# Performance work log

Measured on AMD Instinct MI355X. Metric: run time of the kernel, lower is better.

## Reference

```python
import jax, jax.numpy as jnp
import numpy as np

R = 32          # voxel resolution (init kwarg)
EPS = 0.0       # init kwarg eps


def _norm_coords(coords):
    # coords: [B, 3, N]
    nc = coords - coords.mean(axis=2, keepdims=True)
    # L2 norm over xyz (dim=1), max over points (dim=2)
    denom = jnp.linalg.norm(nc, axis=1, keepdims=True).max(axis=2, keepdims=True) * 2.0 + EPS
    nc = nc / denom + 0.5
    return jnp.clip(nc * R, 0.0, R - 1)  # [B, 3, N] in [0, R-1]


def setup_inputs() -> dict:
    key = jax.random.key(0)
    k1, k2 = jax.random.split(key)
    features = jax.random.normal(k1, (8, 64, 65536), dtype=jnp.float32)
    coords = jax.random.normal(k2, (8, 3, 65536), dtype=jnp.float32)
    return {"features": features, "coords": coords}


def reference(features, coords):
    # features: [B, C, N], coords: [B, 3, N]
    nc = _norm_coords(coords)
    vox = jnp.round(nc).astype(jnp.int32)                      # [B, 3, N]
    flat = (vox[:, 0] * R + vox[:, 1]) * R + vox[:, 2]         # [B, N] flat voxel ids

    def per_batch(f, idx):
        # f: [C, N], idx: [N] -> scatter-mean into R^3 voxels
        sums = jax.ops.segment_sum(f.T, idx, num_segments=R ** 3)            # [R^3, C]
        cnt = jax.ops.segment_sum(jnp.ones(idx.shape, jnp.float32), idx,
                                  num_segments=R ** 3)                        # [R^3]
        return (sums / jnp.maximum(cnt, 1.0)[:, None]).T                      # [C, R^3]

    vox_feat = jax.vmap(per_batch)(features, flat)             # [B, C, R^3]
    B, C = features.shape[0], features.shape[1]
    return vox_feat.reshape(B, C, R, R, R), nc
```

## Files before the change

kernel.cpp:

```cpp
#include <hip/hip_runtime.h>
#include <hip/hip_fp16.h>

#define RR 32
#define R3 32768
#define NPTS 65536
#define NCH 64
#define NB 8


__global__ void mean1_kernel(const float* __restrict__ coords, double* __restrict__ part) {
    __shared__ double ls[3][4];
    int b = blockIdx.y, blk = blockIdx.x;
    int t = threadIdx.x;
    const float* cb = coords + (size_t)b * 3 * NPTS;
    int base = blk * 1024 + t;
    double sx = 0.0, sy = 0.0, sz = 0.0;
#pragma unroll
    for (int k = 0; k < 4; k++) {
        int n = base + k * 256;
        sx += cb[n];
        sy += cb[NPTS + n];
        sz += cb[2 * NPTS + n];
    }
    for (int off = 32; off > 0; off >>= 1) {
        sx += __shfl_down(sx, off);
        sy += __shfl_down(sy, off);
        sz += __shfl_down(sz, off);
    }
    int wave = t >> 6;
    if ((t & 63) == 0) { ls[0][wave] = sx; ls[1][wave] = sy; ls[2][wave] = sz; }
    __syncthreads();
    if (t == 0) {
        part[((size_t)b * 64 + blk) * 3 + 0] = ls[0][0] + ls[0][1] + ls[0][2] + ls[0][3];
        part[((size_t)b * 64 + blk) * 3 + 1] = ls[1][0] + ls[1][1] + ls[1][2] + ls[1][3];
        part[((size_t)b * 64 + blk) * 3 + 2] = ls[2][0] + ls[2][1] + ls[2][2] + ls[2][3];
    }
}

__global__ void mean2_kernel(const double* __restrict__ part, float* __restrict__ meanf) {
    int b = blockIdx.x, l = threadIdx.x;
    double sx = part[((size_t)b * 64 + l) * 3 + 0];
    double sy = part[((size_t)b * 64 + l) * 3 + 1];
    double sz = part[((size_t)b * 64 + l) * 3 + 2];
    for (int off = 32; off > 0; off >>= 1) {
        sx += __shfl_down(sx, off);
        sy += __shfl_down(sy, off);
        sz += __shfl_down(sz, off);
    }
    if (l == 0) {
        meanf[b * 4 + 0] = (float)(sx * (1.0 / NPTS));
        meanf[b * 4 + 1] = (float)(sy * (1.0 / NPTS));
        meanf[b * 4 + 2] = (float)(sz * (1.0 / NPTS));
    }
}

__global__ void max1_kernel(const float* __restrict__ coords,
                            const float* __restrict__ meanf,
                            float* __restrict__ partmax) {
    __shared__ float ls[4];
    int b = blockIdx.y, blk = blockIdx.x;
    int t = threadIdx.x;
    float mx = meanf[b * 4 + 0], my = meanf[b * 4 + 1], mz = meanf[b * 4 + 2];
    const float* cb = coords + (size_t)b * 3 * NPTS;
    int base = blk * 1024 + t;
    float m = 0.0f;
#pragma unroll
    for (int k = 0; k < 4; k++) {
        int n = base + k * 256;
        float dx = cb[n] - mx;
        float dy = cb[NPTS + n] - my;
        float dz = cb[2 * NPTS + n] - mz;
        m = fmaxf(m, dx * dx + dy * dy + dz * dz);
    }
    for (int off = 32; off > 0; off >>= 1) m = fmaxf(m, __shfl_down(m, off));
    int wave = t >> 6;
    if ((t & 63) == 0) ls[wave] = m;
    __syncthreads();
    if (t == 0) partmax[b * 64 + blk] = fmaxf(fmaxf(ls[0], ls[1]), fmaxf(ls[2], ls[3]));
}

__global__ void max2_kernel(const float* __restrict__ partmax, float* __restrict__ denom) {
    int b = blockIdx.x, l = threadIdx.x;
    float m = partmax[b * 64 + l];
    for (int off = 32; off > 0; off >>= 1) m = fmaxf(m, __shfl_down(m, off));
    if (l == 0) denom[b] = 2.0f * sqrtf(m);
}


__global__ void nc_vid_kernel(const float* __restrict__ coords,
                              const float* __restrict__ meanf,
                              const float* __restrict__ denomv,
                              float* __restrict__ ncout,
                              int* __restrict__ vid,
                              unsigned* __restrict__ cnt) {
    int b = blockIdx.y;
    int n = blockIdx.x * blockDim.x + threadIdx.x;
    float mx = meanf[b * 4 + 0], my = meanf[b * 4 + 1], mz = meanf[b * 4 + 2];
    float denom = denomv[b];
    const float* cb = coords + (size_t)b * 3 * NPTS;
    float dx = cb[n] - mx;
    float dy = cb[NPTS + n] - my;
    float dz = cb[2 * NPTS + n] - mz;
    float qx = fminf(fmaxf((dx / denom + 0.5f) * 32.0f, 0.0f), 31.0f);
    float qy = fminf(fmaxf((dy / denom + 0.5f) * 32.0f, 0.0f), 31.0f);
    float qz = fminf(fmaxf((dz / denom + 0.5f) * 32.0f, 0.0f), 31.0f);
    float* nb_ = ncout + (size_t)b * 3 * NPTS;
    nb_[n] = qx;
    nb_[NPTS + n] = qy;
    nb_[2 * NPTS + n] = qz;
    int flat = ((int)rintf(qx) * RR + (int)rintf(qy)) * RR + (int)rintf(qz);
    vid[b * NPTS + n] = flat;
    atomicAdd(&cnt[b * R3 + flat], 1u);
}

__global__ __launch_bounds__(1024) void scan_kernel(const unsigned* __restrict__ cnt,
                                                    unsigned* __restrict__ cursor) {
    __shared__ unsigned buf[R3 + R3 / 32];
    __shared__ unsigned ls[1024];
    int b = blockIdx.x;
    int t = threadIdx.x;
    const unsigned* c = cnt + b * R3;
    for (int i = t; i < R3; i += 1024) buf[i + (i >> 5)] = c[i];
    __syncthreads();
    int sb = t * 33;
    unsigned v[32];
    unsigned s = 0;
#pragma unroll
    for (int k = 0; k < 32; k++) {
        unsigned x = buf[sb + k];
        v[k] = s;
        s += x;
    }
    ls[t] = s;
    __syncthreads();
    for (int d = 1; d < 1024; d <<= 1) {
        unsigned x = (t >= d) ? ls[t - d] : 0u;
        __syncthreads();
        ls[t] += x;
        __syncthreads();
    }
    unsigned chunk_excl = (t == 0) ? 0u : ls[t - 1];
#pragma unroll
    for (int k = 0; k < 32; k++) buf[sb + k] = chunk_excl + v[k];
    __syncthreads();
    unsigned* cur = cursor + b * R3;
    for (int i = t; i < R3; i += 1024) cur[i] = buf[i + (i >> 5)];
}

__global__ void permute_kernel(const float* __restrict__ feats,
                               const int* __restrict__ vid,
                               unsigned* __restrict__ cursor,
                               __half* __restrict__ ft,
                               int* __restrict__ vid_sorted) {
    __shared__ float tile[64][65];
    __shared__ int spos[64];
    int b  = blockIdx.y;
    int n0 = blockIdx.x * 64;
    int t  = threadIdx.x;

    if (t < 64) {
        int flat = vid[b * NPTS + n0 + t];
        int pos = (int)atomicAdd(&cursor[b * R3 + flat], 1u);
        spos[t] = pos;
        vid_sorted[b * NPTS + pos] = flat;
    }

    const float* fb = feats + (size_t)b * NCH * NPTS + n0;
    int i  = t & 63;
    int c0 = t >> 6;
#pragma unroll
    for (int iter = 0; iter < 16; iter++) {
        int c = iter * 4 + c0;
        tile[i][c] = fb[(size_t)c * NPTS + i];
    }
    __syncthreads();

    int wave = t >> 6;
    int lane = t & 63;
    __half* fbase = ft + (size_t)b * NPTS * NCH + lane;
#pragma unroll
    for (int k = 0; k < 16; k++) {
        int p = wave * 16 + k;
        fbase[(size_t)spos[p] * NCH] = __float2half(tile[p][lane]);
    }
}

__global__ void segsum_kernel(const __half* __restrict__ ft,
                              const int* __restrict__ vid_sorted,
                              float* __restrict__ ws_vox) {
    int b    = blockIdx.y;
    int t    = threadIdx.x;
    int wave = t >> 6;
    int lane = t & 63;
    int p0   = (blockIdx.x * 4 + wave) * 64;
    int pend = p0 + 64;
    const int* vs = vid_sorted + (size_t)b * NPTS;

    int p  = p0;
    int v0 = vs[p0];
    if (p0 > 0 && vs[p0 - 1] == v0) {
        while (p < pend && vs[p] == v0) ++p;
        if (p == pend) return;
    }

    const __half* fb = ft + (size_t)b * NPTS * NCH + lane;
    float* wv = ws_vox + (size_t)b * R3 * NCH + lane;

    float s = 0.0f;
    int vcur = vs[p];
    for (;;) {
        s += __half2float(fb[(size_t)p * NCH]);
        ++p;
        int vnext = (p < NPTS) ? vs[p] : -1;
        if (vnext != vcur) {
            wv[(size_t)vcur * NCH] = s;
            if (p >= pend) break;
            s = 0.0f;
            vcur = vnext;
        }
    }
}

__global__ void normalize_t_kernel(const float* __restrict__ ws_vox,
                                   const unsigned* __restrict__ cnt,
                                   float* __restrict__ voxout) {
    __shared__ float tile[64][65];
    __shared__ float cinv[64];
    __shared__ unsigned scnt[64];
    int b  = blockIdx.y;
    int v0 = blockIdx.x * 64;
    int t  = threadIdx.x;
    if (t < 64) {
        unsigned c = cnt[b * R3 + v0 + t];
        scnt[t] = c;
        cinv[t] = 1.0f / fmaxf((float)c, 1.0f);
    }
    __syncthreads();
    const float* src = ws_vox + ((size_t)b * R3 + v0) * NCH;
    int c = t & 63;
    int w = t >> 6;
#pragma unroll
    for (int iter = 0; iter < 16; iter++) {
        int vi = iter * 4 + w;
        tile[c][vi] = scnt[vi] ? src[(size_t)vi * NCH + c] * cinv[vi] : 0.0f;
    }
    __syncthreads();
    float* dst = voxout + (size_t)b * NCH * R3 + v0;
    int vi = t & 63;
#pragma unroll
    for (int iter = 0; iter < 16; iter++) {
        int cc = iter * 4 + w;
        dst[(size_t)cc * R3 + vi] = tile[cc][vi];
    }
}


__global__ void scatter_vm_kernel(const float* __restrict__ feats,
                                  const float* __restrict__ coords,
                                  const float* __restrict__ meanf,
                                  const float* __restrict__ denomv,
                                  float* __restrict__ ws_vox,
                                  float* __restrict__ ncout,
                                  float* __restrict__ cnt) {
    __shared__ float tile[64][65];
    __shared__ int   sflat[64];
    int b  = blockIdx.y;
    int n0 = blockIdx.x * 64;
    int t  = threadIdx.x;
    if (t < 64) {
        int n = n0 + t;
        float mx = meanf[b * 4 + 0], my = meanf[b * 4 + 1], mz = meanf[b * 4 + 2];
        float denom = denomv[b];
        const float* cb = coords + (size_t)b * 3 * NPTS;
        float dx = cb[n] - mx;
        float dy = cb[NPTS + n] - my;
        float dz = cb[2 * NPTS + n] - mz;
        float qx = fminf(fmaxf((dx / denom + 0.5f) * 32.0f, 0.0f), 31.0f);
        float qy = fminf(fmaxf((dy / denom + 0.5f) * 32.0f, 0.0f), 31.0f);
        float qz = fminf(fmaxf((dz / denom + 0.5f) * 32.0f, 0.0f), 31.0f);
        float* nb_ = ncout + (size_t)b * 3 * NPTS;
        nb_[n] = qx;
        nb_[NPTS + n] = qy;
        nb_[2 * NPTS + n] = qz;
        int flat = ((int)rintf(qx) * RR + (int)rintf(qy)) * RR + (int)rintf(qz);
        sflat[t] = flat;
        atomicAdd(&cnt[b * R3 + flat], 1.0f);
    }
    const float* fb = feats + (size_t)b * NCH * NPTS + n0;
    int i = t & 63;
    int c0 = t >> 6;
#pragma unroll
    for (int iter = 0; iter < 16; iter++) {
        int c = iter * 4 + c0;
        tile[i][c] = fb[(size_t)c * NPTS + i];
    }
    __syncthreads();
    int wave = t >> 6;
    int lane = t & 63;
#pragma unroll
    for (int k = 0; k < 16; k++) {
        int p = wave * 16 + k;
        float v = tile[p][lane];
        size_t base = ((size_t)b * R3 + sflat[p]) * NCH;
        atomicAdd(&ws_vox[base + lane], v);
    }
}

__global__ void normalize_tf_kernel(const float* __restrict__ ws_vox,
                                    const float* __restrict__ cnt,
                                    float* __restrict__ voxout) {
    __shared__ float tile[64][65];
    __shared__ float cinv[64];
    int b  = blockIdx.y;
    int v0 = blockIdx.x * 64;
    int t  = threadIdx.x;
    if (t < 64) cinv[t] = 1.0f / fmaxf(cnt[b * R3 + v0 + t], 1.0f);
    __syncthreads();
    const float* src = ws_vox + ((size_t)b * R3 + v0) * NCH;
    int c = t & 63;
    int w = t >> 6;
#pragma unroll
    for (int iter = 0; iter < 16; iter++) {
        int vi = iter * 4 + w;
        tile[c][vi] = src[(size_t)vi * NCH + c] * cinv[vi];
    }
    __syncthreads();
    float* dst = voxout + (size_t)b * NCH * R3 + v0;
    int vi = t & 63;
#pragma unroll
    for (int iter = 0; iter < 16; iter++) {
        int cc = iter * 4 + w;
        dst[(size_t)cc * R3 + vi] = tile[cc][vi];
    }
}

extern "C" void kernel_launch(void* const* d_in, const int* in_sizes, int n_in,
                              void* d_out, int out_size, void* d_ws, size_t ws_size,
                              hipStream_t stream) {
    const float* feats  = (const float*)d_in[0];
    const float* coords = (const float*)d_in[1];
    float* out = (float*)d_out;
    float* voxout = out;
    float* ncout  = out + (size_t)NB * NCH * R3;

    double* part    = (double*)d_ws;
    float*  partmax = (float*)((char*)d_ws + 12544);
    float*  meanf   = (float*)((char*)d_ws + 14592);
    float*  denomv  = (float*)((char*)d_ws + 14720);

    const size_t off_cnt   = 16384;
    const size_t cnt_bytes = (size_t)NB * R3 * 4;
    const size_t off_vox   = off_cnt + cnt_bytes;
    const size_t vox_bytes = (size_t)NB * R3 * NCH * 4;
    const size_t off_cur   = off_vox + vox_bytes;
    const size_t off_vid   = off_cur + cnt_bytes;
    const size_t vid_bytes = (size_t)NB * NPTS * 4;
    const size_t off_vs    = off_vid + vid_bytes;
    const size_t off_ft    = off_vs + vid_bytes;
    const size_t ft_bytes  = (size_t)NB * NPTS * NCH * 2;
    const size_t need_sort = off_ft + ft_bytes;
    const size_t need_vm   = off_vox + vox_bytes;

    if (ws_size >= need_sort) {
        unsigned* cnt    = (unsigned*)((char*)d_ws + off_cnt);
        float*    ws_vox = (float*)((char*)d_ws + off_vox);
        unsigned* cursor = (unsigned*)((char*)d_ws + off_cur);
        int*      vid    = (int*)((char*)d_ws + off_vid);
        int*      vid_s  = (int*)((char*)d_ws + off_vs);
        __half*   ft     = (__half*)((char*)d_ws + off_ft);

        hipMemsetAsync((char*)d_ws + off_cnt, 0, cnt_bytes, stream);

        mean1_kernel<<<dim3(64, NB), 256, 0, stream>>>(coords, part);
        mean2_kernel<<<NB, 64, 0, stream>>>(part, meanf);
        max1_kernel <<<dim3(64, NB), 256, 0, stream>>>(coords, meanf, partmax);
        max2_kernel <<<NB, 64, 0, stream>>>(partmax, denomv);
        nc_vid_kernel<<<dim3(NPTS / 256, NB), 256, 0, stream>>>(coords, meanf, denomv,
                                                                ncout, vid, cnt);
        scan_kernel  <<<NB, 1024, 0, stream>>>(cnt, cursor);
        permute_kernel<<<dim3(NPTS / 64, NB), 256, 0, stream>>>(feats, vid, cursor, ft, vid_s);
        segsum_kernel <<<dim3(NPTS / 256, NB), 256, 0, stream>>>(ft, vid_s, ws_vox);
        normalize_t_kernel<<<dim3(R3 / 64, NB), 256, 0, stream>>>(ws_vox, cnt, voxout);
    } else if (ws_size >= need_vm) {
        float* cntf   = (float*)((char*)d_ws + off_cnt);
        float* ws_vox = (float*)((char*)d_ws + off_vox);
        hipMemsetAsync((char*)d_ws + off_cnt, 0, cnt_bytes + vox_bytes, stream);
        mean1_kernel<<<dim3(64, NB), 256, 0, stream>>>(coords, part);
        mean2_kernel<<<NB, 64, 0, stream>>>(part, meanf);
        max1_kernel <<<dim3(64, NB), 256, 0, stream>>>(coords, meanf, partmax);
        max2_kernel <<<NB, 64, 0, stream>>>(partmax, denomv);
        scatter_vm_kernel<<<dim3(NPTS / 64, NB), 256, 0, stream>>>(
            feats, coords, meanf, denomv, ws_vox, ncout, cntf);
        normalize_tf_kernel<<<dim3(R3 / 64, NB), 256, 0, stream>>>(ws_vox, cntf, voxout);
    }
}
```

Baseline: 393.1 us.

## Split segment-sum into fixed per-wave chunks with preloaded features and atomics

Each wave now sums a fixed 64-point slice of the sorted features, instead of skipping to the first run it owns and walking an unbounded run. Voxel ids for the block are staged in shared memory, and all 64 half-precision rows are loaded into registers up front so many loads are in flight at once. Partial sums at slice boundaries are combined with float atomicAdd, which removes the serial latency-bound walk. In exchange, the voxel accumulator buffer must be zeroed by an extra large memset, and atomics add traffic plus a non-deterministic summation order.

```diff
diff --git a/kernel.cpp b/kernel.cpp
--- a/kernel.cpp
+++ b/kernel.cpp
@@ -188,37 +188,40 @@
 __global__ void segsum_kernel(const __half* __restrict__ ft,
                               const int* __restrict__ vid_sorted,
                               float* __restrict__ ws_vox) {
+    __shared__ int svid[257];
     int b    = blockIdx.y;
     int t    = threadIdx.x;
     int wave = t >> 6;
     int lane = t & 63;
-    int p0   = (blockIdx.x * 4 + wave) * 64;
-    int pend = p0 + 64;
-    const int* vs = vid_sorted + (size_t)b * NPTS;
-
-    int p  = p0;
-    int v0 = vs[p0];
-    if (p0 > 0 && vs[p0 - 1] == v0) {
-        while (p < pend && vs[p] == v0) ++p;
-        if (p == pend) return;
-    }
-
-    const __half* fb = ft + (size_t)b * NPTS * NCH + lane;
+    int bp0  = blockIdx.x * 256;
+
+    svid[t] = vid_sorted[b * NPTS + bp0 + t];
+    if (t == 0)
+        svid[256] = (bp0 + 256 < NPTS) ? vid_sorted[b * NPTS + bp0 + 256] : -1;
+    __syncthreads();
+
+    int p0 = wave * 64;
+    const __half* fb = ft + ((size_t)b * NPTS + bp0 + p0) * NCH + lane;
     float* wv = ws_vox + (size_t)b * R3 * NCH + lane;
 
+    float v[64];
+#pragma unroll
+    for (int k = 0; k < 64; k++) v[k] = __half2float(fb[(size_t)k * NCH]);
+
     float s = 0.0f;
-    int vcur = vs[p];
-    for (;;) {
-        s += __half2float(fb[(size_t)p * NCH]);
-        ++p;
-        int vnext = (p < NPTS) ? vs[p] : -1;
+    int vcur = svid[p0];
+#pragma unroll
+    for (int k = 0; k < 64; k++) {
+        s += v[k];
+        int vnext = svid[p0 + k + 1];
+        if (k == 63 && wave == 3) vnext = svid[256];
         if (vnext != vcur) {
-            wv[(size_t)vcur * NCH] = s;
-            if (p >= pend) break;
+            atomicAdd(wv + (size_t)vcur * NCH, s);
             s = 0.0f;
             vcur = vnext;
         }
     }
+    if (s != 0.0f) atomicAdd(wv + (size_t)vcur * NCH, s);
 }
 
 __global__ void normalize_t_kernel(const float* __restrict__ ws_vox,
@@ -369,7 +372,7 @@
         int*      vid_s  = (int*)((char*)d_ws + off_vs);
         __half*   ft     = (__half*)((char*)d_ws + off_ft);
 
-        hipMemsetAsync((char*)d_ws + off_cnt, 0, cnt_bytes, stream);
+        hipMemsetAsync((char*)d_ws + off_cnt, 0, cnt_bytes + vox_bytes, stream);
 
         mean1_kernel<<<dim3(64, NB), 256, 0, stream>>>(coords, part);
         mean2_kernel<<<NB, 64, 0, stream>>>(part, meanf);
```

Result: faster. 329.9 us (-16.1%).
